# Kernel optimization log

Hardware: AMD Instinct MI355X
Metric: run time of the kernel (lower is better)

## Reference

```python
import jax, jax.numpy as jnp
import numpy as np

H = 16       # num_heads
HD = 64      # head_dim = embed_dim // num_heads
CLIP = 64    # clipping_threshold (Shaw et al. k)
B, L, D = 4, 1024, 1024


def setup_inputs() -> dict:
    key = jax.random.key(0)
    ks = jax.random.split(key, 13)
    f = lambda k_, s: jax.random.normal(k_, s, dtype=jnp.float32) * 0.02
    return {
        "q": f(ks[0], (B, L, D)),
        "k": f(ks[1], (B, L, D)),
        "v": f(ks[2], (B, L, D)),
        "Wq": f(ks[3], (D, D)), "bq": jnp.zeros((D,), jnp.float32),
        "Wk": f(ks[4], (D, D)), "bk": jnp.zeros((D,), jnp.float32),
        "Wv": f(ks[5], (D, D)), "bv": jnp.zeros((D,), jnp.float32),
        "Wo": f(ks[6], (D, D)), "bo": jnp.zeros((D,), jnp.float32),
        "Ek": f(ks[7], (2 * CLIP + 1, HD)),  # relative_position_k table
        "Ev": f(ks[8], (2 * CLIP + 1, HD)),  # relative_position_v table
    }


def reference(q, k, v, Wq, bq, Wk, bk, Wv, bv, Wo, bo, Ek, Ev):
    b, lq, d = q.shape
    lk = k.shape[1]
    # input projections (torch Linear: x @ W^T + b)
    qp = (q @ Wq.T + bq).reshape(b, lq, H, HD)
    kp = (k @ Wk.T + bk).reshape(b, lk, H, HD)
    vp = (v @ Wv.T + bv).reshape(b, lk, H, HD)
    # content-content scores
    attn1 = jnp.einsum("bqhd,bkhd->bhqk", qp, kp)
    # relative position embeddings R: (lq, lk, HD)
    idx = jnp.clip(jnp.arange(lk)[None, :] - jnp.arange(lq)[:, None], -CLIP, CLIP) + CLIP
    rel_k = Ek[idx]
    rel_v = Ev[idx]
    # content-position scores (Shaw et al. term added to QK^T)
    attn2 = jnp.einsum("bqhd,qkd->bhqk", qp, rel_k)
    scale = jnp.sqrt(jnp.asarray(HD, dtype=q.dtype))
    attn = jax.nn.softmax((attn1 + attn2) / scale, axis=-1)  # (b,H,lq,lk)
    # weighted values + relative value term
    out1 = jnp.einsum("bhqk,bkhd->bqhd", attn, vp)
    out2 = jnp.einsum("bhqk,qkd->bqhd", attn, rel_v)
    out = (out1 + out2).reshape(b, lq, d)
    return out @ Wo.T + bo
```

## Files before the change

### kernel.cpp

```cpp
#include <hip/hip_runtime.h>
#include <hip/hip_bf16.h>
#include <stdint.h>
#include <stddef.h>

#define B_ 4
#define L_ 1024
#define D_ 1024
#define H_ 16
#define HD_ 64
#define NROW 65536
#define QE_LD 132
#define EV_LD 192
#define T_STR 200

typedef __attribute__((ext_vector_type(8))) short bf16x8;
typedef __attribute__((ext_vector_type(4))) float f32x4;
typedef __attribute__((ext_vector_type(4))) unsigned short u16x4;

__device__ __forceinline__ float bf2f(unsigned short u) {
  union { unsigned int i; float f; } v; v.i = ((unsigned int)u) << 16; return v.f;
}
__device__ __forceinline__ unsigned short f2bf(float f) {
  union { float f; unsigned int i; } v; v.f = f;
  return (unsigned short)((v.i + 0x7fffu + ((v.i >> 16) & 1u)) >> 16);
}
__device__ __forceinline__ unsigned short f2bfrn(float f) {
  __hip_bfloat16 h = __float2bfloat16(f);
  return *reinterpret_cast<unsigned short*>(&h);
}
__device__ __forceinline__ void async16(const void* g, void* l) {
  __builtin_amdgcn_global_load_lds(
      (const __attribute__((address_space(1))) unsigned int*)g,
      (__attribute__((address_space(3))) unsigned int*)l, 16, 0, 0);
}

struct ConvArgs7 { const float* s[7]; unsigned short* d[7]; int n4[7]; };

__global__ __launch_bounds__(256) void f32_to_bf16_multi(ConvArgs7 a) {
  const int y = blockIdx.y;
  const float* s = a.s[y];
  unsigned short* d = a.d[y];
  const int n4 = a.n4[y];
  int i = blockIdx.x * 256 + threadIdx.x;
  int stride = gridDim.x * 256;
  for (; i < n4; i += stride) {
    float4 v = ((const float4*)s)[i];
    u16x4 o;
    o[0] = f2bf(v.x); o[1] = f2bf(v.y); o[2] = f2bf(v.z); o[3] = f2bf(v.w);
    ((u16x4*)d)[i] = o;
  }
}

__global__ __launch_bounds__(256) void build_ekev_k(const float* __restrict__ Ek,
                                                    const float* __restrict__ Ev,
                                                    unsigned short* __restrict__ Ekp,
                                                    unsigned short* __restrict__ EvTp) {
  int i = blockIdx.x * 256 + threadIdx.x;
  if (i < 256 * 64) {
    int r = i >> 6, dd = i & 63;
    Ekp[i] = (r < 129) ? f2bf(Ek[r * 64 + dd]) : (unsigned short)0;
  }
  if (i < 128 * EV_LD) {
    int dd = i / EV_LD, r = i - dd * EV_LD;
    EvTp[i] = (dd < 64 && r < 129) ? f2bf(Ev[r * 64 + dd]) : (unsigned short)0;
  }
}

struct Gemm3 {
  const unsigned short* A[3];
  const unsigned short* Bt[3];
  const float* bias[3];
  void* C[3];
};

template<int MI, bool OBF16, bool BIAS>
__global__ __launch_bounds__(256, 4) void gemm_bt(Gemm3 ga, int lda, int ldb, int ldc,
                                                  int Ncut, int ktiles) {
  constexpr int BM = MI * 32;
  constexpr int AI = MI / 2;
  __shared__ unsigned short Al[2][BM * 32];
  __shared__ unsigned short Bl[2][128 * 32];
  const unsigned short* A = ga.A[blockIdx.z];
  const unsigned short* Bt = ga.Bt[blockIdx.z];
  const float* bias = ga.bias[blockIdx.z];
  void* Cv = ga.C[blockIdx.z];
  const int tid = threadIdx.x;
  const int w = tid >> 6, l = tid & 63;
  const int l15 = l & 15, lg = l >> 4;
  const int row0 = blockIdx.x * BM, col0 = blockIdx.y * 128;
  const int wm = (w >> 1) * (MI * 16), wn = (w & 1) * 64;

  f32x4 acc[MI][4];
#pragma unroll
  for (int i = 0; i < MI; ++i)
#pragma unroll
    for (int j = 0; j < 4; ++j) acc[i][j] = {0.f, 0.f, 0.f, 0.f};

  auto stage = [&](int buf, int kt) {
#pragma unroll
    for (int i = 0; i < AI; ++i) {
      int p = (i * 4 + w) * 1024 + l * 16;
      int m = p >> 6;
      int clog = (l & 3) ^ ((m >> 1) & 3);
      async16(A + (size_t)(row0 + m) * lda + kt * 32 + clog * 8,
              (char*)&Al[buf][0] + (i * 4 + w) * 1024);
    }
#pragma unroll
    for (int i = 0; i < 2; ++i) {
      int p = (i * 4 + w) * 1024 + l * 16;
      int m = p >> 6;
      int clog = (l & 3) ^ ((m >> 1) & 3);
      async16(Bt + (size_t)(col0 + m) * ldb + kt * 32 + clog * 8,
              (char*)&Bl[buf][0] + (i * 4 + w) * 1024);
    }
  };

  stage(0, 0);
  __syncthreads();
  for (int kt = 0; kt < ktiles; ++kt) {
    int cur = kt & 1;
    if (kt + 1 < ktiles) stage(cur ^ 1, kt + 1);
    bf16x8 af[MI], bfr[4];
#pragma unroll
    for (int mi = 0; mi < MI; ++mi) {
      int m = wm + mi * 16 + l15;
      af[mi] = *(const bf16x8*)&Al[cur][m * 32 + ((lg ^ ((m >> 1) & 3)) << 3)];
    }
#pragma unroll
    for (int ni = 0; ni < 4; ++ni) {
      int n = wn + ni * 16 + l15;
      bfr[ni] = *(const bf16x8*)&Bl[cur][n * 32 + ((lg ^ ((n >> 1) & 3)) << 3)];
    }
#pragma unroll
    for (int mi = 0; mi < MI; ++mi)
#pragma unroll
      for (int ni = 0; ni < 4; ++ni)
        acc[mi][ni] = __builtin_amdgcn_mfma_f32_16x16x32_bf16(af[mi], bfr[ni], acc[mi][ni], 0, 0, 0);
    __syncthreads();
  }

#pragma unroll
  for (int ni = 0; ni < 4; ++ni) {
    int col = col0 + wn + ni * 16 + l15;
    if (col < Ncut) {
      float bv = BIAS ? bias[col] : 0.f;
#pragma unroll
      for (int mi = 0; mi < MI; ++mi) {
        int rowb = row0 + wm + mi * 16 + lg * 4;
#pragma unroll
        for (int r = 0; r < 4; ++r) {
          float v = acc[mi][ni][r] + bv;
          size_t off = (size_t)(rowb + r) * ldc + col;
          if (OBF16) ((unsigned short*)Cv)[off] = f2bf(v);
          else       ((float*)Cv)[off] = v;
        }
      }
    }
  }
}

__global__ __launch_bounds__(256) void transpose_v_k(const unsigned short* __restrict__ vp,
                                                     unsigned short* __restrict__ vpT) {
  const int lt = blockIdx.x, bh = blockIdx.y;
  const int b = bh >> 4, h = bh & 15;
  __shared__ unsigned short tile[64][72];
  const int t = threadIdx.x;
#pragma unroll
  for (int j = 0; j < 2; ++j) {
    int lrow = (t >> 3) + 32 * j;
    int d0 = (t & 7) * 8;
    bf16x8 v = *(const bf16x8*)(vp + ((size_t)((b * L_ + lt * 64 + lrow) * H_ + h)) * HD_ + d0);
#pragma unroll
    for (int e = 0; e < 8; ++e) tile[lrow][d0 + e] = (unsigned short)v[e];
  }
  __syncthreads();
#pragma unroll
  for (int j = 0; j < 2; ++j) {
    int d = (t >> 3) + 32 * j;
    int l0 = (t & 7) * 8;
    bf16x8 o;
#pragma unroll
    for (int e = 0; e < 8; ++e) o[e] = (short)tile[l0 + e][d];
    *(bf16x8*)(vpT + ((size_t)((b * H_ + h) * HD_ + d)) * L_ + lt * 64 + l0) = o;
  }
}

__global__ __launch_bounds__(256, 4) void flash_fwd_k(
    const unsigned short* __restrict__ qp, const unsigned short* __restrict__ kp,
    const unsigned short* __restrict__ vpT, const unsigned short* __restrict__ qE,
    const unsigned short* __restrict__ EvTp, unsigned short* __restrict__ tmp) {
  __shared__ __align__(16) char smem[32768];
  unsigned short (*Kl)[4096] = (unsigned short (*)[4096])smem;
  unsigned short (*Vl)[4096] = (unsigned short (*)[4096])(smem + 16384);
  const int tid = threadIdx.x, w = tid >> 6, l = tid & 63;
  const int l15 = l & 15, lg = l >> 4;
  const int bid = blockIdx.x;
  const int bh = bid & 63, qt = bid >> 6;
  const int b = bh >> 4, h = bh & 15;
  const int qw = qt * 64 + w * 16;
  const int q_lane = qw + l15;
  const int rowbase = (b * L_ + qw) * H_ + h;
  const int rowi_lane = rowbase + l15 * H_;
  constexpr float C1 = 0.125f * 1.44269504f;

  bf16x8 qf[2];
  {
    const unsigned short* qrp = qp + (size_t)rowi_lane * HD_;
#pragma unroll
    for (int ks = 0; ks < 2; ++ks) qf[ks] = *(const bf16x8*)(qrp + ks * 32 + lg * 8);
  }
  const unsigned short* qerow = qE + (size_t)rowi_lane * QE_LD;
  const float qe0L = bf2f(qerow[0]) * C1;
  const float qe128L = bf2f(qerow[128]) * C1;

  f32x4 O[4];
#pragma unroll
  for (int nd = 0; nd < 4; ++nd) O[nd] = {0.f, 0.f, 0.f, 0.f};
  float mrow = -1e30f, lrow = 0.f, t0row = 0.f;

  u16x4 pks0[4], pks1[4], pks2[4];
  float mu0 = -1e30f, mu1 = -1e30f, mu2 = -1e30f;
  {
    u16x4 z4 = {0, 0, 0, 0};
#pragma unroll
    for (int ni = 0; ni < 4; ++ni) { pks0[ni] = z4; pks1[ni] = z4; pks2[ni] = z4; }
  }

  auto stage = [&](int buf, int kt) {
#pragma unroll
    for (int i = 0; i < 2; ++i) {
      int p = (i * 4 + w) * 1024 + l * 16;
      int row = p >> 7;
      int clog = (l & 7) ^ (row & 7);
      async16(kp + ((size_t)((b * L_ + kt * 64 + row) * H_ + h)) * HD_ + clog * 8,
              (char*)&Kl[buf][0] + (i * 4 + w) * 1024);
      async16(vpT + ((size_t)((b * H_ + h) * HD_ + row)) * L_ + kt * 64 + clog * 8,
              (char*)&Vl[buf][0] + (i * 4 + w) * 1024);
    }
  };

  stage(0, 0);
  __syncthreads();

  for (int kt = 0; kt < 16; ++kt) {
    int cur = kt & 1;
    if (kt + 1 < 16) stage(cur ^ 1, kt + 1);

    f32x4 S[4];
#pragma unroll
    for (int ni = 0; ni < 4; ++ni) S[ni] = {0.f, 0.f, 0.f, 0.f};
#pragma unroll
    for (int ks = 0; ks < 2; ++ks) {
      bf16x8 kf[4];
#pragma unroll
      for (int ni = 0; ni < 4; ++ni) {
        int kk = ni * 16 + l15;
        kf[ni] = *(const bf16x8*)&Kl[cur][kk * 64 + (((ks * 4 + lg) ^ (kk & 7)) << 3)];
      }
#pragma unroll
      for (int ni = 0; ni < 4; ++ni)
        S[ni] = __builtin_amdgcn_mfma_f32_16x16x32_bf16(kf[ni], qf[ks], S[ni], 0, 0, 0);
    }

    const int cls = (kt <= qt - 2) ? 0 : ((kt >= qt + 2) ? 2 : 1);
    const int based = kt * 64 - q_lane;

    if (cls == 1) {
#pragma unroll
      for (int ni = 0; ni < 4; ++ni)
#pragma unroll
        for (int r = 0; r < 4; ++r) {
          int delta = based + ni * 16 + lg * 4 + r;
          int idx = min(max(delta, -64), 64) + 64;
          S[ni][r] = S[ni][r] * C1 + bf2f(qerow[idx]) * C1;
        }
    } else {
      float qeL = (cls == 0) ? qe0L : qe128L;
#pragma unroll
      for (int ni = 0; ni < 4; ++ni)
#pragma unroll
        for (int r = 0; r < 4; ++r) S[ni][r] = S[ni][r] * C1 + qeL;
    }

    float x0 = fmaxf(fmaxf(S[0][0], S[0][1]), fmaxf(S[0][2], S[0][3]));
    float x1 = fmaxf(fmaxf(S[1][0], S[1][1]), fmaxf(S[1][2], S[1][3]));
    float x2 = fmaxf(fmaxf(S[2][0], S[2][1]), fmaxf(S[2][2], S[2][3]));
    float x3 = fmaxf(fmaxf(S[3][0], S[3][1]), fmaxf(S[3][2], S[3][3]));
    float pmax = fmaxf(fmaxf(x0, x1), fmaxf(x2, x3));
    pmax = fmaxf(pmax, __shfl_xor(pmax, 16));
    pmax = fmaxf(pmax, __shfl_xor(pmax, 32));

    float a = 1.f;
    if (!__all(pmax <= mrow + 11.54f)) {
      float mnew = fmaxf(mrow, pmax);
      a = __builtin_amdgcn_exp2f(mrow - mnew);
      mrow = mnew;
      float aq0 = __shfl(a, lg * 4 + 0);
      float aq1 = __shfl(a, lg * 4 + 1);
      float aq2 = __shfl(a, lg * 4 + 2);
      float aq3 = __shfl(a, lg * 4 + 3);
#pragma unroll
      for (int nd = 0; nd < 4; ++nd) {
        O[nd][0] *= aq0; O[nd][1] *= aq1; O[nd][2] *= aq2; O[nd][3] *= aq3;
      }
    }

#pragma unroll
    for (int ni = 0; ni < 4; ++ni)
#pragma unroll
      for (int r = 0; r < 4; ++r)
        S[ni][r] = __builtin_amdgcn_exp2f(S[ni][r] - mrow);

    float s0 = (S[0][0] + S[0][1]) + (S[0][2] + S[0][3]);
    float s1 = (S[1][0] + S[1][1]) + (S[1][2] + S[1][3]);
    float s2 = (S[2][0] + S[2][1]) + (S[2][2] + S[2][3]);
    float s3 = (S[3][0] + S[3][1]) + (S[3][2] + S[3][3]);
    float ps = (s0 + s1) + (s2 + s3);
    ps += __shfl_xor(ps, 16);
    ps += __shfl_xor(ps, 32);
    lrow = lrow * a + ps;

    if (cls == 0) {
      t0row = t0row * a + ps;
    } else if (cls == 2) {
      t0row = t0row * a;
    } else if (kt == qt - 1) {
      float p0 = 0.f;
#pragma unroll
      for (int ni = 0; ni < 4; ++ni)
#pragma unroll
        for (int r = 0; r < 4; ++r)
          if (based + ni * 16 + lg * 4 + r <= -64) p0 += S[ni][r];
      p0 += __shfl_xor(p0, 16);
      p0 += __shfl_xor(p0, 32);
      t0row = t0row * a + p0;
    } else {
      t0row = t0row * a;
    }

    asm volatile("" ::: "memory");
    __builtin_amdgcn_s_barrier();
    asm volatile("" ::: "memory");
    unsigned short* Plw = (unsigned short*)(smem + cur * 8192) + w * 1024;

    u16x4 pcur[4];
#pragma unroll
    for (int ni = 0; ni < 4; ++ni) {
      u16x4 pk;
#pragma unroll
      for (int r = 0; r < 4; ++r) pk[r] = f2bfrn(S[ni][r]);
      pcur[ni] = pk;
      int slot = (ni * 2 + (lg >> 1)) ^ (l15 & 7);
      int addr = l15 * 64 + (slot << 3) + (lg & 1) * 4;
      *(u16x4*)&Plw[addr] = pk;
    }
    if (cls == 1) {
      if (kt == qt - 1) {
#pragma unroll
        for (int ni = 0; ni < 4; ++ni) pks0[ni] = pcur[ni];
        mu0 = mrow;
      } else if (kt == qt) {
#pragma unroll
        for (int ni = 0; ni < 4; ++ni) pks1[ni] = pcur[ni];
        mu1 = mrow;
      } else {
#pragma unroll
        for (int ni = 0; ni < 4; ++ni) pks2[ni] = pcur[ni];
        mu2 = mrow;
      }
    }

#pragma unroll
    for (int ks = 0; ks < 2; ++ks) {
      bf16x8 pf = *(const bf16x8*)&Plw[l15 * 64 + (((ks * 4 + lg) ^ (l15 & 7)) << 3)];
      bf16x8 vf[4];
#pragma unroll
      for (int nd = 0; nd < 4; ++nd) {
        int d = nd * 16 + l15;
        vf[nd] = *(const bf16x8*)&Vl[cur][d * 64 + (((ks * 4 + lg) ^ (d & 7)) << 3)];
      }
#pragma unroll
      for (int nd = 0; nd < 4; ++nd)
        O[nd] = __builtin_amdgcn_mfma_f32_16x16x32_bf16(pf, vf[nd], O[nd], 0, 0, 0);
    }
    __syncthreads();
  }

  unsigned short* Tl16 = (unsigned short*)smem + w * (16 * T_STR);
  {
    u16x4 z4 = {0, 0, 0, 0};
    u16x4* tl4 = (u16x4*)Tl16;
    for (int i = l; i < 16 * T_STR / 4; i += 64) tl4[i] = z4;
  }
  float bandsum = 0.f;
  auto addband = [&](const u16x4* pk, float muv, int btc) {
    float scale = __builtin_amdgcn_exp2f(muv - mrow);
    int jbase = (qt + btc - 1) * 64 + lg * 4 - q_lane + 64;
#pragma unroll
    for (int ni = 0; ni < 4; ++ni)
#pragma unroll
      for (int r = 0; r < 4; ++r) {
        int j = jbase + ni * 16 + r;
        if (j >= 1 && j <= 127) {
          float pf = bf2f((unsigned short)pk[ni][r]) * scale;
          Tl16[l15 * T_STR + j] = f2bfrn(pf);
          bandsum += pf;
        }
      }
  };
  addband(pks0, mu0, 0);
  addband(pks1, mu1, 1);
  addband(pks2, mu2, 2);
  bandsum += __shfl_xor(bandsum, 16);
  bandsum += __shfl_xor(bandsum, 32);
  if (lg == 0) {
    Tl16[l15 * T_STR] = f2bfrn(t0row);
    Tl16[l15 * T_STR + 128] = f2bfrn(fmaxf(0.f, lrow - t0row - bandsum));
  }
#pragma unroll
  for (int ks6 = 0; ks6 < 6; ++ks6) {
    bf16x8 af = *(const bf16x8*)(Tl16 + l15 * T_STR + ks6 * 32 + lg * 8);
    bf16x8 bfr[4];
#pragma unroll
    for (int nd = 0; nd < 4; ++nd)
      bfr[nd] = *(const bf16x8*)(EvTp + (size_t)(nd * 16 + l15) * EV_LD + ks6 * 32 + lg * 8);
#pragma unroll
    for (int nd = 0; nd < 4; ++nd)
      O[nd] = __builtin_amdgcn_mfma_f32_16x16x32_bf16(af, bfr[nd], O[nd], 0, 0, 0);
  }

  float invl = 1.f / lrow;
  float iq[4];
#pragma unroll
  for (int r = 0; r < 4; ++r) iq[r] = __shfl(invl, lg * 4 + r);
#pragma unroll
  for (int r = 0; r < 4; ++r) {
    size_t rowi = (size_t)(rowbase + (lg * 4 + r) * H_);
#pragma unroll
    for (int nd = 0; nd < 4; ++nd)
      tmp[rowi * HD_ + nd * 16 + l15] = f2bfrn(O[nd][r] * iq[r]);
  }
}

extern "C" void kernel_launch(void* const* d_in, const int* in_sizes, int n_in,
                              void* d_out, int out_size, void* d_ws, size_t ws_size,
                              hipStream_t stream) {
  (void)in_sizes; (void)n_in; (void)out_size; (void)ws_size;
  const float* q  = (const float*)d_in[0];
  const float* k  = (const float*)d_in[1];
  const float* v  = (const float*)d_in[2];
  const float* Wq = (const float*)d_in[3];
  const float* bq = (const float*)d_in[4];
  const float* Wk = (const float*)d_in[5];
  const float* bk = (const float*)d_in[6];
  const float* Wv = (const float*)d_in[7];
  const float* bv = (const float*)d_in[8];
  const float* Wo = (const float*)d_in[9];
  const float* bo = (const float*)d_in[10];
  const float* Ek = (const float*)d_in[11];
  const float* Ev = (const float*)d_in[12];

  char* ws = (char*)d_ws;
  constexpr size_t SZ_QKV = (size_t)B_ * L_ * D_ * 2;
  constexpr size_t SZ_W   = (size_t)D_ * D_ * 2;
  constexpr size_t OFF_QB = 0;
  constexpr size_t OFF_KB = OFF_QB + SZ_QKV;
  constexpr size_t OFF_VB = OFF_KB + SZ_QKV;
  constexpr size_t OFF_WQ = OFF_VB + SZ_QKV;
  constexpr size_t OFF_WK = OFF_WQ + SZ_W;
  constexpr size_t OFF_WV = OFF_WK + SZ_W;
  constexpr size_t OFF_WO = OFF_WV + SZ_W;
  constexpr size_t OFF_EKP = OFF_WO + SZ_W;
  constexpr size_t OFF_EVT = OFF_EKP + 256 * 64 * 2;
  constexpr size_t OFF_QE = OFF_EVT + 128 * EV_LD * 2;
  constexpr size_t OFF_QP = OFF_QE + (size_t)NROW * QE_LD * 2;
  constexpr size_t OFF_KP = OFF_QP + SZ_QKV;
  constexpr size_t OFF_VP = OFF_KP + SZ_QKV;
  constexpr size_t OFF_VPT = OFF_VP + SZ_QKV;
  constexpr size_t OFF_TMP = OFF_VPT + SZ_QKV;

  auto U16 = [&](size_t off) { return (unsigned short*)(ws + off); };

  {
    ConvArgs7 c{};
    c.s[0] = q;  c.d[0] = U16(OFF_QB); c.n4[0] = (B_ * L_ * D_) / 4;
    c.s[1] = k;  c.d[1] = U16(OFF_KB); c.n4[1] = (B_ * L_ * D_) / 4;
    c.s[2] = v;  c.d[2] = U16(OFF_VB); c.n4[2] = (B_ * L_ * D_) / 4;
    c.s[3] = Wq; c.d[3] = U16(OFF_WQ); c.n4[3] = (D_ * D_) / 4;
    c.s[4] = Wk; c.d[4] = U16(OFF_WK); c.n4[4] = (D_ * D_) / 4;
    c.s[5] = Wv; c.d[5] = U16(OFF_WV); c.n4[5] = (D_ * D_) / 4;
    c.s[6] = Wo; c.d[6] = U16(OFF_WO); c.n4[6] = (D_ * D_) / 4;
    f32_to_bf16_multi<<<dim3(1024, 7), 256, 0, stream>>>(c);
  }
  build_ekev_k<<<96, 256, 0, stream>>>(Ek, Ev, U16(OFF_EKP), U16(OFF_EVT));

  {
    Gemm3 g{};
    g.A[0] = U16(OFF_QB); g.Bt[0] = U16(OFF_WQ); g.bias[0] = bq; g.C[0] = U16(OFF_QP);
    g.A[1] = U16(OFF_KB); g.Bt[1] = U16(OFF_WK); g.bias[1] = bk; g.C[1] = U16(OFF_KP);
    g.A[2] = U16(OFF_VB); g.Bt[2] = U16(OFF_WV); g.bias[2] = bv; g.C[2] = U16(OFF_VP);
    gemm_bt<2, true, true><<<dim3(64, 8, 3), 256, 0, stream>>>(g, 1024, 1024, 1024, 1024, 32);
  }

  transpose_v_k<<<dim3(16, 64), 256, 0, stream>>>(U16(OFF_VP), U16(OFF_VPT));

  {
    Gemm3 g{};
    g.A[0] = U16(OFF_QP); g.Bt[0] = U16(OFF_EKP); g.bias[0] = nullptr; g.C[0] = U16(OFF_QE);
    gemm_bt<2, true, false><<<dim3(1024, 2, 1), 256, 0, stream>>>(g, 64, 64, QE_LD, 129, 2);
  }

  flash_fwd_k<<<1024, 256, 0, stream>>>(
      U16(OFF_QP), U16(OFF_KP), U16(OFF_VPT), U16(OFF_QE), U16(OFF_EVT), U16(OFF_TMP));

  {
    Gemm3 g{};
    g.A[0] = U16(OFF_TMP); g.Bt[0] = U16(OFF_WO); g.bias[0] = bo; g.C[0] = d_out;
    gemm_bt<2, false, true><<<dim3(64, 8, 1), 256, 0, stream>>>(g, 1024, 1024, 1024, 1024, 32);
  }
}
```

Baseline: 154.1 us.

## Fuse fp32-to-bf16 conversion into GEMM tile loads, drop separate cast kernel

Removes the standalone kernel that cast q, k, v and the weight matrices to bf16. The GEMM now loads fp32 tiles straight into registers, converts them, and writes them to LDS in the swizzled layout. This avoids one full read and write pass over about 60 MB of activations and weights plus a kernel launch. In exchange, the fp32 path uses register-staged synchronous loads instead of async global-to-LDS copies. The weights are also re-read and re-converted by every row block, which raises global traffic on the B side.

```diff
diff --git a/kernel.cpp b/kernel.cpp
--- a/kernel.cpp
+++ b/kernel.cpp
@@ -34,23 +34,6 @@
       (__attribute__((address_space(3))) unsigned int*)l, 16, 0, 0);
 }
 
-struct ConvArgs7 { const float* s[7]; unsigned short* d[7]; int n4[7]; };
-
-__global__ __launch_bounds__(256) void f32_to_bf16_multi(ConvArgs7 a) {
-  const int y = blockIdx.y;
-  const float* s = a.s[y];
-  unsigned short* d = a.d[y];
-  const int n4 = a.n4[y];
-  int i = blockIdx.x * 256 + threadIdx.x;
-  int stride = gridDim.x * 256;
-  for (; i < n4; i += stride) {
-    float4 v = ((const float4*)s)[i];
-    u16x4 o;
-    o[0] = f2bf(v.x); o[1] = f2bf(v.y); o[2] = f2bf(v.z); o[3] = f2bf(v.w);
-    ((u16x4*)d)[i] = o;
-  }
-}
-
 __global__ __launch_bounds__(256) void build_ekev_k(const float* __restrict__ Ek,
                                                     const float* __restrict__ Ev,
                                                     unsigned short* __restrict__ Ekp,
@@ -67,21 +50,23 @@
 }
 
 struct Gemm3 {
-  const unsigned short* A[3];
-  const unsigned short* Bt[3];
+  const void* A[3];
+  const void* Bt[3];
   const float* bias[3];
   void* C[3];
 };
 
-template<int MI, bool OBF16, bool BIAS>
+struct ARegs { float4 v0, v1; };
+struct BRegs { float4 v0, v1, v2, v3; };
+
+template<int MI, bool AF32, bool BF32, bool OBF16, bool BIAS>
 __global__ __launch_bounds__(256, 4) void gemm_bt(Gemm3 ga, int lda, int ldb, int ldc,
                                                   int Ncut, int ktiles) {
   constexpr int BM = MI * 32;
-  constexpr int AI = MI / 2;
   __shared__ unsigned short Al[2][BM * 32];
   __shared__ unsigned short Bl[2][128 * 32];
-  const unsigned short* A = ga.A[blockIdx.z];
-  const unsigned short* Bt = ga.Bt[blockIdx.z];
+  const void* Av = ga.A[blockIdx.z];
+  const void* Btv = ga.Bt[blockIdx.z];
   const float* bias = ga.bias[blockIdx.z];
   void* Cv = ga.C[blockIdx.z];
   const int tid = threadIdx.x;
@@ -89,6 +74,7 @@
   const int l15 = l & 15, lg = l >> 4;
   const int row0 = blockIdx.x * BM, col0 = blockIdx.y * 128;
   const int wm = (w >> 1) * (MI * 16), wn = (w & 1) * 64;
+  const int idx = w * 64 + l;
 
   f32x4 acc[MI][4];
 #pragma unroll
@@ -96,30 +82,78 @@
 #pragma unroll
     for (int j = 0; j < 4; ++j) acc[i][j] = {0.f, 0.f, 0.f, 0.f};
 
-  auto stage = [&](int buf, int kt) {
-#pragma unroll
-    for (int i = 0; i < AI; ++i) {
+  auto agload = [&](int buf, int kt) {
+#pragma unroll
+    for (int i = 0; i < MI / 2; ++i) {
       int p = (i * 4 + w) * 1024 + l * 16;
       int m = p >> 6;
       int clog = (l & 3) ^ ((m >> 1) & 3);
-      async16(A + (size_t)(row0 + m) * lda + kt * 32 + clog * 8,
+      async16((const unsigned short*)Av + (size_t)(row0 + m) * lda + kt * 32 + clog * 8,
               (char*)&Al[buf][0] + (i * 4 + w) * 1024);
     }
+  };
+  auto bgload = [&](int buf, int kt) {
 #pragma unroll
     for (int i = 0; i < 2; ++i) {
       int p = (i * 4 + w) * 1024 + l * 16;
       int m = p >> 6;
       int clog = (l & 3) ^ ((m >> 1) & 3);
-      async16(Bt + (size_t)(col0 + m) * ldb + kt * 32 + clog * 8,
+      async16((const unsigned short*)Btv + (size_t)(col0 + m) * ldb + kt * 32 + clog * 8,
               (char*)&Bl[buf][0] + (i * 4 + w) * 1024);
     }
   };
-
-  stage(0, 0);
+  auto aload = [&](ARegs& r, int kt) {
+    int am = idx >> 2, ac = idx & 3;
+    const float* ap = (const float*)Av + (size_t)(row0 + am) * lda + kt * 32 + ac * 8;
+    r.v0 = *(const float4*)ap;
+    r.v1 = *(const float4*)(ap + 4);
+  };
+  auto astore = [&](const ARegs& r, int buf) {
+    int am = idx >> 2, ac = idx & 3;
+    bf16x8 o;
+    o[0] = (short)f2bfrn(r.v0.x); o[1] = (short)f2bfrn(r.v0.y);
+    o[2] = (short)f2bfrn(r.v0.z); o[3] = (short)f2bfrn(r.v0.w);
+    o[4] = (short)f2bfrn(r.v1.x); o[5] = (short)f2bfrn(r.v1.y);
+    o[6] = (short)f2bfrn(r.v1.z); o[7] = (short)f2bfrn(r.v1.w);
+    *(bf16x8*)&Al[buf][am * 32 + ((ac ^ ((am >> 1) & 3)) << 3)] = o;
+  };
+  auto bload = [&](BRegs& r, int kt) {
+    int bn = idx >> 1, bh2 = idx & 1;
+    const float* bp = (const float*)Btv + (size_t)(col0 + bn) * ldb + kt * 32 + bh2 * 16;
+    r.v0 = *(const float4*)bp;
+    r.v1 = *(const float4*)(bp + 4);
+    r.v2 = *(const float4*)(bp + 8);
+    r.v3 = *(const float4*)(bp + 12);
+  };
+  auto bstore = [&](const BRegs& r, int buf) {
+    int bn = idx >> 1, bh2 = idx & 1;
+    int c0 = bh2 * 2, c1 = bh2 * 2 + 1;
+    bf16x8 o0, o1;
+    o0[0] = (short)f2bfrn(r.v0.x); o0[1] = (short)f2bfrn(r.v0.y);
+    o0[2] = (short)f2bfrn(r.v0.z); o0[3] = (short)f2bfrn(r.v0.w);
+    o0[4] = (short)f2bfrn(r.v1.x); o0[5] = (short)f2bfrn(r.v1.y);
+    o0[6] = (short)f2bfrn(r.v1.z); o0[7] = (short)f2bfrn(r.v1.w);
+    o1[0] = (short)f2bfrn(r.v2.x); o1[1] = (short)f2bfrn(r.v2.y);
+    o1[2] = (short)f2bfrn(r.v2.z); o1[3] = (short)f2bfrn(r.v2.w);
+    o1[4] = (short)f2bfrn(r.v3.x); o1[5] = (short)f2bfrn(r.v3.y);
+    o1[6] = (short)f2bfrn(r.v3.z); o1[7] = (short)f2bfrn(r.v3.w);
+    *(bf16x8*)&Bl[buf][bn * 32 + ((c0 ^ ((bn >> 1) & 3)) << 3)] = o0;
+    *(bf16x8*)&Bl[buf][bn * 32 + ((c1 ^ ((bn >> 1) & 3)) << 3)] = o1;
+  };
+
+  ARegs ar; BRegs br;
+  if (AF32) { aload(ar, 0); } else { agload(0, 0); }
+  if (BF32) { bload(br, 0); } else { bgload(0, 0); }
+  if (AF32) { astore(ar, 0); }
+  if (BF32) { bstore(br, 0); }
   __syncthreads();
+
   for (int kt = 0; kt < ktiles; ++kt) {
     int cur = kt & 1;
-    if (kt + 1 < ktiles) stage(cur ^ 1, kt + 1);
+    if (kt + 1 < ktiles) {
+      if (AF32) { aload(ar, kt + 1); } else { agload(cur ^ 1, kt + 1); }
+      if (BF32) { bload(br, kt + 1); } else { bgload(cur ^ 1, kt + 1); }
+    }
     bf16x8 af[MI], bfr[4];
 #pragma unroll
     for (int mi = 0; mi < MI; ++mi) {
@@ -136,6 +170,10 @@
 #pragma unroll
       for (int ni = 0; ni < 4; ++ni)
         acc[mi][ni] = __builtin_amdgcn_mfma_f32_16x16x32_bf16(af[mi], bfr[ni], acc[mi][ni], 0, 0, 0);
+    if (kt + 1 < ktiles) {
+      if (AF32) { astore(ar, cur ^ 1); }
+      if (BF32) { bstore(br, cur ^ 1); }
+    }
     __syncthreads();
   }
 
@@ -462,15 +500,7 @@
 
   char* ws = (char*)d_ws;
   constexpr size_t SZ_QKV = (size_t)B_ * L_ * D_ * 2;
-  constexpr size_t SZ_W   = (size_t)D_ * D_ * 2;
-  constexpr size_t OFF_QB = 0;
-  constexpr size_t OFF_KB = OFF_QB + SZ_QKV;
-  constexpr size_t OFF_VB = OFF_KB + SZ_QKV;
-  constexpr size_t OFF_WQ = OFF_VB + SZ_QKV;
-  constexpr size_t OFF_WK = OFF_WQ + SZ_W;
-  constexpr size_t OFF_WV = OFF_WK + SZ_W;
-  constexpr size_t OFF_WO = OFF_WV + SZ_W;
-  constexpr size_t OFF_EKP = OFF_WO + SZ_W;
+  constexpr size_t OFF_EKP = 0;
   constexpr size_t OFF_EVT = OFF_EKP + 256 * 64 * 2;
   constexpr size_t OFF_QE = OFF_EVT + 128 * EV_LD * 2;
   constexpr size_t OFF_QP = OFF_QE + (size_t)NROW * QE_LD * 2;
@@ -481,25 +511,15 @@
 
   auto U16 = [&](size_t off) { return (unsigned short*)(ws + off); };
 
-  {
-    ConvArgs7 c{};
-    c.s[0] = q;  c.d[0] = U16(OFF_QB); c.n4[0] = (B_ * L_ * D_) / 4;
-    c.s[1] = k;  c.d[1] = U16(OFF_KB); c.n4[1] = (B_ * L_ * D_) / 4;
-    c.s[2] = v;  c.d[2] = U16(OFF_VB); c.n4[2] = (B_ * L_ * D_) / 4;
-    c.s[3] = Wq; c.d[3] = U16(OFF_WQ); c.n4[3] = (D_ * D_) / 4;
-    c.s[4] = Wk; c.d[4] = U16(OFF_WK); c.n4[4] = (D_ * D_) / 4;
-    c.s[5] = Wv; c.d[5] = U16(OFF_WV); c.n4[5] = (D_ * D_) / 4;
-    c.s[6] = Wo; c.d[6] = U16(OFF_WO); c.n4[6] = (D_ * D_) / 4;
-    f32_to_bf16_multi<<<dim3(1024, 7), 256, 0, stream>>>(c);
-  }
   build_ekev_k<<<96, 256, 0, stream>>>(Ek, Ev, U16(OFF_EKP), U16(OFF_EVT));
 
   {
     Gemm3 g{};
-    g.A[0] = U16(OFF_QB); g.Bt[0] = U16(OFF_WQ); g.bias[0] = bq; g.C[0] = U16(OFF_QP);
-    g.A[1] = U16(OFF_KB); g.Bt[1] = U16(OFF_WK); g.bias[1] = bk; g.C[1] = U16(OFF_KP);
-    g.A[2] = U16(OFF_VB); g.Bt[2] = U16(OFF_WV); g.bias[2] = bv; g.C[2] = U16(OFF_VP);
-    gemm_bt<2, true, true><<<dim3(64, 8, 3), 256, 0, stream>>>(g, 1024, 1024, 1024, 1024, 32);
+    g.A[0] = q; g.Bt[0] = Wq; g.bias[0] = bq; g.C[0] = U16(OFF_QP);
+    g.A[1] = k; g.Bt[1] = Wk; g.bias[1] = bk; g.C[1] = U16(OFF_KP);
+    g.A[2] = v; g.Bt[2] = Wv; g.bias[2] = bv; g.C[2] = U16(OFF_VP);
+    gemm_bt<2, true, true, true, true><<<dim3(64, 8, 3), 256, 0, stream>>>(
+        g, 1024, 1024, 1024, 1024, 32);
   }
 
   transpose_v_k<<<dim3(16, 64), 256, 0, stream>>>(U16(OFF_VP), U16(OFF_VPT));
@@ -507,7 +527,8 @@
   {
     Gemm3 g{};
     g.A[0] = U16(OFF_QP); g.Bt[0] = U16(OFF_EKP); g.bias[0] = nullptr; g.C[0] = U16(OFF_QE);
-    gemm_bt<2, true, false><<<dim3(1024, 2, 1), 256, 0, stream>>>(g, 64, 64, QE_LD, 129, 2);
+    gemm_bt<2, false, false, true, false><<<dim3(1024, 2, 1), 256, 0, stream>>>(
+        g, 64, 64, QE_LD, 129, 2);
   }
 
   flash_fwd_k<<<1024, 256, 0, stream>>>(
@@ -515,7 +536,8 @@
 
   {
     Gemm3 g{};
-    g.A[0] = U16(OFF_TMP); g.Bt[0] = U16(OFF_WO); g.bias[0] = bo; g.C[0] = d_out;
-    gemm_bt<2, false, true><<<dim3(64, 8, 1), 256, 0, stream>>>(g, 1024, 1024, 1024, 1024, 32);
-  }
-}
+    g.A[0] = U16(OFF_TMP); g.Bt[0] = Wo; g.bias[0] = bo; g.C[0] = d_out;
+    gemm_bt<2, false, true, false, true><<<dim3(64, 8, 1), 256, 0, stream>>>(
+        g, 1024, 1024, 1024, 1024, 32);
+  }
+}
```

Measured after the change: 189.2 us. 22.8% more time.

## Fuse V transpose into QKV projection epilogue and enlarge QKV GEMM tile

Applied to the files above, without the earlier changes.

The QKV projection GEMM now writes the V output directly in head-transposed layout (b,h,d,l) from its epilogue, so the separate transpose kernel and the intermediate vp buffer go away. The QKV GEMM also switches to a 128-row tile (MI=4), with launch bounds derived from MI. This removes one launch and a full read and write of V, at the cost of 8-byte strided stores in the V epilogue and fewer blocks on the projection.

```diff
diff --git a/kernel.cpp b/kernel.cpp
--- a/kernel.cpp
+++ b/kernel.cpp
@@ -73,11 +73,10 @@
   void* C[3];
 };
 
-template<int MI, bool OBF16, bool BIAS>
-__global__ __launch_bounds__(256, 4) void gemm_bt(Gemm3 ga, int lda, int ldb, int ldc,
-                                                  int Ncut, int ktiles) {
+template<int MI, bool OBF16, bool BIAS, bool VPT>
+__global__ __launch_bounds__(256, 8 / MI) void gemm_bt(Gemm3 ga, int lda, int ldb, int ldc,
+                                                       int Ncut, int ktiles) {
   constexpr int BM = MI * 32;
-  constexpr int AI = MI / 2;
   __shared__ unsigned short Al[2][BM * 32];
   __shared__ unsigned short Bl[2][128 * 32];
   const unsigned short* A = ga.A[blockIdx.z];
@@ -98,7 +97,7 @@
 
   auto stage = [&](int buf, int kt) {
 #pragma unroll
-    for (int i = 0; i < AI; ++i) {
+    for (int i = 0; i < MI / 2; ++i) {
       int p = (i * 4 + w) * 1024 + l * 16;
       int m = p >> 6;
       int clog = (l & 3) ^ ((m >> 1) & 3);
@@ -139,6 +138,25 @@
     __syncthreads();
   }
 
+  if (VPT && blockIdx.z == 2) {
+    unsigned short* vpT = (unsigned short*)Cv;
+#pragma unroll
+    for (int ni = 0; ni < 4; ++ni) {
+      int col = col0 + wn + ni * 16 + l15;
+      float bv = BIAS ? bias[col] : 0.f;
+#pragma unroll
+      for (int mi = 0; mi < MI; ++mi) {
+        int rowb = row0 + wm + mi * 16 + lg * 4;
+        int bb = rowb >> 10, lrow = rowb & 1023;
+        u16x4 o;
+#pragma unroll
+        for (int r = 0; r < 4; ++r) o[r] = f2bf(acc[mi][ni][r] + bv);
+        *(u16x4*)(vpT + ((size_t)((bb * H_ + (col >> 6)) * HD_ + (col & 63))) * L_ + lrow) = o;
+      }
+    }
+    return;
+  }
+
 #pragma unroll
   for (int ni = 0; ni < 4; ++ni) {
     int col = col0 + wn + ni * 16 + l15;
@@ -156,32 +174,6 @@
         }
       }
     }
-  }
-}
-
-__global__ __launch_bounds__(256) void transpose_v_k(const unsigned short* __restrict__ vp,
-                                                     unsigned short* __restrict__ vpT) {
-  const int lt = blockIdx.x, bh = blockIdx.y;
-  const int b = bh >> 4, h = bh & 15;
-  __shared__ unsigned short tile[64][72];
-  const int t = threadIdx.x;
-#pragma unroll
-  for (int j = 0; j < 2; ++j) {
-    int lrow = (t >> 3) + 32 * j;
-    int d0 = (t & 7) * 8;
-    bf16x8 v = *(const bf16x8*)(vp + ((size_t)((b * L_ + lt * 64 + lrow) * H_ + h)) * HD_ + d0);
-#pragma unroll
-    for (int e = 0; e < 8; ++e) tile[lrow][d0 + e] = (unsigned short)v[e];
-  }
-  __syncthreads();
-#pragma unroll
-  for (int j = 0; j < 2; ++j) {
-    int d = (t >> 3) + 32 * j;
-    int l0 = (t & 7) * 8;
-    bf16x8 o;
-#pragma unroll
-    for (int e = 0; e < 8; ++e) o[e] = (short)tile[l0 + e][d];
-    *(bf16x8*)(vpT + ((size_t)((b * H_ + h) * HD_ + d)) * L_ + lt * 64 + l0) = o;
   }
 }
 
@@ -475,8 +467,7 @@
   constexpr size_t OFF_QE = OFF_EVT + 128 * EV_LD * 2;
   constexpr size_t OFF_QP = OFF_QE + (size_t)NROW * QE_LD * 2;
   constexpr size_t OFF_KP = OFF_QP + SZ_QKV;
-  constexpr size_t OFF_VP = OFF_KP + SZ_QKV;
-  constexpr size_t OFF_VPT = OFF_VP + SZ_QKV;
+  constexpr size_t OFF_VPT = OFF_KP + SZ_QKV;
   constexpr size_t OFF_TMP = OFF_VPT + SZ_QKV;
 
   auto U16 = [&](size_t off) { return (unsigned short*)(ws + off); };
@@ -498,16 +489,16 @@
     Gemm3 g{};
     g.A[0] = U16(OFF_QB); g.Bt[0] = U16(OFF_WQ); g.bias[0] = bq; g.C[0] = U16(OFF_QP);
     g.A[1] = U16(OFF_KB); g.Bt[1] = U16(OFF_WK); g.bias[1] = bk; g.C[1] = U16(OFF_KP);
-    g.A[2] = U16(OFF_VB); g.Bt[2] = U16(OFF_WV); g.bias[2] = bv; g.C[2] = U16(OFF_VP);
-    gemm_bt<2, true, true><<<dim3(64, 8, 3), 256, 0, stream>>>(g, 1024, 1024, 1024, 1024, 32);
-  }
-
-  transpose_v_k<<<dim3(16, 64), 256, 0, stream>>>(U16(OFF_VP), U16(OFF_VPT));
+    g.A[2] = U16(OFF_VB); g.Bt[2] = U16(OFF_WV); g.bias[2] = bv; g.C[2] = U16(OFF_VPT);
+    gemm_bt<4, true, true, true><<<dim3(32, 8, 3), 256, 0, stream>>>(
+        g, 1024, 1024, 1024, 1024, 32);
+  }
 
   {
     Gemm3 g{};
     g.A[0] = U16(OFF_QP); g.Bt[0] = U16(OFF_EKP); g.bias[0] = nullptr; g.C[0] = U16(OFF_QE);
-    gemm_bt<2, true, false><<<dim3(1024, 2, 1), 256, 0, stream>>>(g, 64, 64, QE_LD, 129, 2);
+    gemm_bt<2, true, false, false><<<dim3(1024, 2, 1), 256, 0, stream>>>(
+        g, 64, 64, QE_LD, 129, 2);
   }
 
   flash_fwd_k<<<1024, 256, 0, stream>>>(
@@ -516,6 +507,7 @@
   {
     Gemm3 g{};
     g.A[0] = U16(OFF_TMP); g.Bt[0] = U16(OFF_WO); g.bias[0] = bo; g.C[0] = d_out;
-    gemm_bt<2, false, true><<<dim3(64, 8, 1), 256, 0, stream>>>(g, 1024, 1024, 1024, 1024, 32);
-  }
-}
+    gemm_bt<2, false, true, false><<<dim3(64, 8, 1), 256, 0, stream>>>(
+        g, 1024, 1024, 1024, 1024, 32);
+  }
+}
```

Measured after the change: 138.5 us. -10.1%, faster.
